# Kernel optimization log

Hardware: AMD Instinct MI355X
Metric: run time of the kernel (lower is better)

Reference implementation:

```python
import jax, jax.numpy as jnp
import numpy as np
import math


def _silu(v):
    return v * jax.nn.sigmoid(v)


def setup_inputs() -> dict:
    key = jax.random.key(0)
    ks = jax.random.split(key, 8)
    b, l = 4, 2048
    dim, hidden, d_state, dt_rank = 1024, 2048, 16, 64
    s = 0.02
    x = jax.random.normal(ks[0], (b, l, dim), dtype=jnp.float32)
    W_in = jax.random.normal(ks[1], (2 * hidden, dim), dtype=jnp.float32) * s
    conv_w = jax.random.normal(ks[2], (hidden, 1, 3), dtype=jnp.float32) * s  # depthwise, k=3
    conv_b = jnp.zeros((hidden,), dtype=jnp.float32)
    W_xproj = jax.random.normal(ks[3], (dt_rank + 2 * d_state, hidden), dtype=jnp.float32) * s
    W_dt = jax.random.uniform(ks[4], (hidden, dt_rank), minval=-1.0 / dt_rank, maxval=1.0 / dt_rank, dtype=jnp.float32)
    dt_init = jnp.exp(jax.random.uniform(ks[5], (hidden,), dtype=jnp.float32) * (math.log(0.1) - math.log(0.001)) + math.log(0.001))
    b_dt = -1.0 / dt_init  # matches dt_proj.bias init in source
    A_log = -jnp.arange(1, d_state + 1, dtype=jnp.float32)
    D = jnp.ones((hidden,), dtype=jnp.float32)
    W_out = jax.random.normal(ks[6], (dim, hidden), dtype=jnp.float32) * s
    return {"x": x, "W_in": W_in, "conv_w": conv_w, "conv_b": conv_b,
            "W_xproj": W_xproj, "W_dt": W_dt, "b_dt": b_dt,
            "A_log": A_log, "D": D, "W_out": W_out}


def reference(x, W_in, conv_w, conv_b, W_xproj, W_dt, b_dt, A_log, D, W_out):
    b, l, dim = x.shape
    hidden = W_dt.shape[0]
    dt_rank = W_dt.shape[1]
    d_state = A_log.shape[0]

    # in_proj and chunk into (x, z)
    xz = jnp.einsum('bld,ed->ble', x, W_in)  # (b, l, 2*hidden)
    u, z = jnp.split(xz, 2, axis=-1)

    # depthwise conv1d, kernel 3, symmetric padding 1 (non-causal, as in source)
    uc = jax.lax.conv_general_dilated(
        jnp.moveaxis(u, 1, 2), conv_w, window_strides=(1,), padding=[(1, 1)],
        dimension_numbers=('NCH', 'OIH', 'NCH'), feature_group_count=hidden)
    uc = jnp.moveaxis(uc + conv_b[None, :, None], 1, 2)  # (b, l, hidden)
    uc = _silu(uc)

    # x_proj -> (dt, B, C)
    x_dbl = jnp.einsum('blh,eh->ble', uc, W_xproj)
    dtp = x_dbl[..., :dt_rank]
    Bm = x_dbl[..., dt_rank:dt_rank + d_state]   # (b, l, n)
    Cm = x_dbl[..., dt_rank + d_state:]          # (b, l, n)
    dt = jax.nn.softplus(jnp.einsum('blr,hr->blh', dtp, W_dt) + b_dt)  # (b, l, hidden)

    A = -jnp.exp(A_log)  # (n,)

    # selective scan: h_{k} = exp(dt_k * A) * h_{k-1} + B_k (outer) u_k ; y_k = C_k . h_k
    def step(h, inp):
        u_t, dt_t, B_t, C_t = inp  # (b,h), (b,h), (b,n), (b,n)
        dA = jnp.exp(dt_t[:, None, :] * A[None, :, None])      # (b, n, h)
        h = dA * h + B_t[:, :, None] * u_t[:, None, :]         # (b, n, h)
        y_t = jnp.einsum('bn,bnh->bh', C_t, h)
        return h, y_t

    xs = (jnp.moveaxis(uc, 0, 1), jnp.moveaxis(dt, 0, 1),
          jnp.moveaxis(Bm, 0, 1), jnp.moveaxis(Cm, 0, 1))
    h0 = jnp.zeros((b, d_state, hidden), dtype=uc.dtype)
    _, ys = jax.lax.scan(step, h0, xs)
    y = jnp.moveaxis(ys, 0, 1) + D * uc  # skip term D*u

    y = y * _silu(z)
    out = jnp.einsum('blh,dh->bld', y, W_out)
    return x + out
```

## Files before the change

### kernel.cpp

```cpp
#include <hip/hip_runtime.h>
#include <cmath>

typedef unsigned short u16;
typedef __bf16 bf16x8 __attribute__((ext_vector_type(8)));
typedef float f32x4 __attribute__((ext_vector_type(4)));
typedef unsigned short u16x8 __attribute__((ext_vector_type(8)));

#define NB_B   4
#define NB_L   2048
#define NB_DIM 1024
#define NB_H   2048
#define NB_NS  16
#define NB_DTR 64
#define NB_TOK (NB_B * NB_L)
#define NCHUNK 64
#define CLEN   32

__device__ __forceinline__ u16 f2b(float f) {
  union { float f; unsigned u; } v; v.f = f;
  unsigned r = v.u + 0x7fffu + ((v.u >> 16) & 1u);
  return (u16)(r >> 16);
}
__device__ __forceinline__ float b2f(u16 h) {
  union { unsigned u; float f; } v; v.u = ((unsigned)h) << 16;
  return v.f;
}
__device__ __forceinline__ float exp_small(float w) {
  return __builtin_fmaf(w, __builtin_fmaf(w, 0.5f, 1.0f), 1.0f);
}

#define CVT_N0 2097152
#define CVT_N1 (CVT_N0 + 1048576)
#define CVT_N2 (CVT_N1 + 32768)
#define CVT_N3 (CVT_N2 + 524288)
__global__ void cvt_all_k(const float* __restrict__ x, const float* __restrict__ W_in,
                          const float* __restrict__ W_dt, const float* __restrict__ W_out,
                          u16* __restrict__ xb, u16* __restrict__ winb,
                          u16* __restrict__ wdtb, u16* __restrict__ woutb) {
  int i = blockIdx.x * 256 + threadIdx.x;
  const float* src; u16* dst; int off;
  if (i < CVT_N0)      { src = x;     dst = xb;    off = i; }
  else if (i < CVT_N1) { src = W_in;  dst = winb;  off = i - CVT_N0; }
  else if (i < CVT_N2) { src = W_dt;  dst = wdtb;  off = i - CVT_N1; }
  else                 { src = W_out; dst = woutb; off = i - CVT_N2; }
  float4 v = reinterpret_cast<const float4*>(src)[off];
  ushort4 o;
  o.x = f2b(v.x); o.y = f2b(v.y); o.z = f2b(v.z); o.w = f2b(v.w);
  reinterpret_cast<ushort4*>(dst)[off] = o;
}

__global__ void cvt_pad_xproj_k(const float* __restrict__ in, u16* __restrict__ out) {
  int i = blockIdx.x * 256 + threadIdx.x;
  int r = i >> 11, c = i & 2047;
  out[i] = (r < 96) ? f2b(in[r * 2048 + c]) : (u16)0;
}

__global__ void extract_dtp_k(const float* __restrict__ xdbl, u16* __restrict__ out) {
  int i = blockIdx.x * 256 + threadIdx.x;
  int r = i >> 6, c = i & 63;
  out[i] = f2b(xdbl[r * 128 + c]);
}

#define EPI_BF16    0
#define EPI_F32     1
#define EPI_SP_BF16 2
#define EPI_RES_F32 3

__device__ __forceinline__ void stage16(const u16* g, u16* l) {
  __builtin_amdgcn_global_load_lds(
      (const __attribute__((address_space(1))) unsigned int*)g,
      (__attribute__((address_space(3))) unsigned int*)l, 16, 0, 0);
}

template <int EPI, int BM>
__global__ __launch_bounds__(512, 1)
void gemm8p_k(const u16* __restrict__ A, const u16* __restrict__ Bm,
              int K, int ldc,
              u16* __restrict__ outB, float* __restrict__ outF,
              const float* __restrict__ bias, const float* __restrict__ resid,
              int cr, int cc, int ncx) {
  constexpr int MR = BM / 32;
  constexpr int MH = MR / 2;
  constexpr int HA = BM / 2;
  constexpr int LA = BM / 128;
  constexpr int L  = 2 * LA + 4;
  constexpr int BUFE = (BM + 256) * 64;
  __shared__ u16 smem[2 * BUFE];

  const int tid  = threadIdx.x;
  const int lane = tid & 63;
  const int wave = tid >> 6;
  const int wr = wave >> 2, wc = wave & 3;
  const int fr = lane & 15, fq = lane >> 4;

  const int bid = blockIdx.x;
  const int e = bid & 7, w = bid >> 3;
  const int row0 = ((e / ncx) * cr + (w % cr)) * BM;
  const int col0 = ((e % ncx) * cc + (w / cr)) * 256;

  f32x4 acc[MR][4] = {};
  bf16x8 bB[4][2], bA0[MH][2], bA1[MH][2];

  auto STAGE_B = [&](int kt) {
    const int k0 = kt * 64;
    u16* base = smem + (kt & 1) * BUFE + BM * 64;
#pragma unroll
    for (int h = 0; h < 2; ++h)
#pragma unroll
      for (int l = 0; l < 2; ++l) {
        int c = l * 512 + tid;
        int rih = c >> 3, p = c & 7;
        stage16(Bm + (size_t)(col0 + h * 128 + rih) * K + k0 + ((p ^ (rih & 7)) * 8),
                base + (h * 128 + rih) * 64 + p * 8);
      }
  };
  auto STAGE_A = [&](int kt) {
    const int k0 = kt * 64;
    u16* base = smem + (kt & 1) * BUFE;
#pragma unroll
    for (int h = 0; h < 2; ++h)
#pragma unroll
      for (int l = 0; l < LA; ++l) {
        int c = l * 512 + tid;
        int rih = c >> 3, p = c & 7;
        stage16(A + (size_t)(row0 + h * HA + rih) * K + k0 + ((p ^ (rih & 7)) * 8),
                base + (h * HA + rih) * 64 + p * 8);
      }
  };
  auto LD_A = [&](int m, int kk, int bi) {
    int rt = wr * HA + m * 16 + fr;
    int p = (kk * 4 + fq) ^ (rt & 7);
    return *reinterpret_cast<const bf16x8*>(smem + bi * BUFE + rt * 64 + p * 8);
  };
  auto LD_B = [&](int n, int kk, int bi) {
    int rt = wc * 64 + n * 16 + fr;
    int p = (kk * 4 + fq) ^ (rt & 7);
    return *reinterpret_cast<const bf16x8*>(smem + bi * BUFE + BM * 64 + rt * 64 + p * 8);
  };

  const int nk = K >> 6;
  STAGE_B(0); STAGE_A(0);
  if (nk > 1) { STAGE_B(1); STAGE_A(1); }
  if (nk > 1) asm volatile("s_waitcnt vmcnt(%0)" :: "i"(L) : "memory");
  else        asm volatile("s_waitcnt vmcnt(0)" ::: "memory");
  __builtin_amdgcn_s_barrier();
  __builtin_amdgcn_sched_barrier(0);
#pragma unroll
  for (int n = 0; n < 4; ++n) { bB[n][0] = LD_B(n, 0, 0); bB[n][1] = LD_B(n, 1, 0); }
#pragma unroll
  for (int m = 0; m < MH; ++m) { bA0[m][0] = LD_A(m, 0, 0); bA0[m][1] = LD_A(m, 1, 0); }
  asm volatile("s_waitcnt lgkmcnt(0)" ::: "memory");
  __builtin_amdgcn_s_barrier();
  __builtin_amdgcn_sched_barrier(0);

  for (int kt = 0; kt < nk; ++kt) {
    const int bi = kt & 1;
    if (kt + 2 < nk) STAGE_B(kt + 2);
    __builtin_amdgcn_s_setprio(1);
#pragma unroll
    for (int m = 0; m < MH; ++m)
#pragma unroll
      for (int n = 0; n < 2; ++n)
#pragma unroll
        for (int kk = 0; kk < 2; ++kk)
          acc[m][n] = __builtin_amdgcn_mfma_f32_16x16x32_bf16(bA0[m][kk], bB[n][kk], acc[m][n], 0, 0, 0);
    __builtin_amdgcn_s_setprio(0);
    __builtin_amdgcn_sched_barrier(0);
#pragma unroll
    for (int m = 0; m < MH; ++m) { bA1[m][0] = LD_A(MH + m, 0, bi); bA1[m][1] = LD_A(MH + m, 1, bi); }
    __builtin_amdgcn_s_setprio(1);
#pragma unroll
    for (int m = 0; m < MH; ++m)
#pragma unroll
      for (int n = 2; n < 4; ++n)
#pragma unroll
        for (int kk = 0; kk < 2; ++kk)
          acc[m][n] = __builtin_amdgcn_mfma_f32_16x16x32_bf16(bA0[m][kk], bB[n][kk], acc[m][n], 0, 0, 0);
    __builtin_amdgcn_s_setprio(0);
    asm volatile("s_waitcnt lgkmcnt(0)" ::: "memory");
    __builtin_amdgcn_s_barrier();
    __builtin_amdgcn_sched_barrier(0);
    if (kt + 2 < nk) STAGE_A(kt + 2);
    __builtin_amdgcn_s_setprio(1);
#pragma unroll
    for (int m = 0; m < MH; ++m)
#pragma unroll
      for (int n = 0; n < 2; ++n)
#pragma unroll
        for (int kk = 0; kk < 2; ++kk)
          acc[MH + m][n] = __builtin_amdgcn_mfma_f32_16x16x32_bf16(bA1[m][kk], bB[n][kk], acc[MH + m][n], 0, 0, 0);
    __builtin_amdgcn_s_setprio(0);
    __builtin_amdgcn_sched_barrier(0);
    if (kt + 1 < nk) {
      if (kt + 2 < nk) asm volatile("s_waitcnt vmcnt(%0)" :: "i"(L) : "memory");
      else             asm volatile("s_waitcnt vmcnt(0)" ::: "memory");
      __builtin_amdgcn_s_barrier();
      __builtin_amdgcn_sched_barrier(0);
#pragma unroll
      for (int n = 0; n < 2; ++n) { bB[n][0] = LD_B(n, 0, bi ^ 1); bB[n][1] = LD_B(n, 1, bi ^ 1); }
#pragma unroll
      for (int m = 0; m < MH; ++m) { bA0[m][0] = LD_A(m, 0, bi ^ 1); bA0[m][1] = LD_A(m, 1, bi ^ 1); }
    }
    __builtin_amdgcn_s_setprio(1);
#pragma unroll
    for (int m = 0; m < MH; ++m)
#pragma unroll
      for (int n = 2; n < 4; ++n)
#pragma unroll
        for (int kk = 0; kk < 2; ++kk)
          acc[MH + m][n] = __builtin_amdgcn_mfma_f32_16x16x32_bf16(bA1[m][kk], bB[n][kk], acc[MH + m][n], 0, 0, 0);
    __builtin_amdgcn_s_setprio(0);
    if (kt + 1 < nk) {
#pragma unroll
      for (int n = 2; n < 4; ++n) { bB[n][0] = LD_B(n, 0, bi ^ 1); bB[n][1] = LD_B(n, 1, bi ^ 1); }
    }
    asm volatile("s_waitcnt lgkmcnt(0)" ::: "memory");
    __builtin_amdgcn_s_barrier();
    __builtin_amdgcn_sched_barrier(0);
  }

  if constexpr (EPI == EPI_BF16 || EPI == EPI_SP_BF16) {
    u16* wv = smem + wave * 1152;
#pragma unroll
    for (int m = 0; m < MR; ++m) {
#pragma unroll
      for (int n = 0; n < 4; ++n) {
        const int c = col0 + wc * 64 + n * 16 + fr;
        float bv = (EPI == EPI_SP_BF16) ? bias[c] : 0.f;
#pragma unroll
        for (int j = 0; j < 4; ++j) {
          float v = acc[m][n][j];
          if (EPI == EPI_SP_BF16) {
            float xx = v + bv;
            float t = __expf(xx);
            float sp = (xx > -5.f) ? log1pf(t) : t;
            v = (xx > 20.f) ? xx : sp;
          }
          wv[(fq * 4 + j) * 72 + n * 16 + fr] = f2b(v);
        }
      }
#pragma unroll
      for (int p = 0; p < 2; ++p) {
        const int rf = p * 8 + (lane >> 3);
        const int c0 = (lane & 7) * 8;
        u16x8 ov = *reinterpret_cast<const u16x8*>(wv + rf * 72 + c0);
        const int grow = row0 + wr * HA + m * 16 + rf;
        const int gcol = col0 + wc * 64 + c0;
        *reinterpret_cast<u16x8*>(&outB[(size_t)grow * ldc + gcol]) = ov;
      }
    }
  } else {
#pragma unroll
    for (int m = 0; m < MR; ++m) {
      const int r = row0 + wr * HA + m * 16 + fq * 4;
#pragma unroll
      for (int n = 0; n < 4; ++n) {
        const int c = col0 + wc * 64 + n * 16 + fr;
#pragma unroll
        for (int j = 0; j < 4; ++j) {
          size_t o = (size_t)(r + j) * ldc + c;
          if (EPI == EPI_F32) outF[o] = acc[m][n][j];
          else                outF[o] = acc[m][n][j] + resid[o];
        }
      }
    }
  }
}

template <int EPI, int BM, int BN>
__global__ __launch_bounds__(256)
void gemm_bt_k(const u16* __restrict__ A, const u16* __restrict__ Bm,
               int K, int ldc,
               u16* __restrict__ outB, float* __restrict__ outF,
               const float* __restrict__ bias, const float* __restrict__ resid) {
  constexpr int MR = BM / 32, NR = BN / 32;
  __shared__ u16 smem[(BM + BN) * 32];
  u16* As = smem;
  u16* Bs = smem + BM * 32;
  const int tid  = threadIdx.x;
  const int lane = tid & 63;
  const int wave = tid >> 6;
  const int wr = wave >> 1, wc = wave & 1;
  const int row0 = blockIdx.x * BM;
  const int col0 = blockIdx.y * BN;
  f32x4 acc[MR][NR] = {};

  const int r_ld = tid >> 2;
  const int kb   = (((tid & 3) ^ ((tid >> 3) & 3)) * 8);
  const size_t a_base = (size_t)(row0 + r_ld) * K + kb;
  const size_t b_base = (size_t)(col0 + r_ld) * K + kb;
  u16* lA = As + tid * 8;
  u16* lB = Bs + tid * 8;

  const int fr = lane & 15;
  const int fq = lane >> 4;
  const int fkx = ((fq ^ ((fr >> 1) & 3)) * 8);

  const int nk = K >> 5;
  for (int kt = 0; kt < nk; ++kt) {
    const int k0 = kt * 32;
    __syncthreads();
#pragma unroll
    for (int hh = 0; hh < BM / 64; ++hh)
      stage16(A + a_base + (size_t)(hh * 64) * K + k0, lA + hh * 64 * 32);
#pragma unroll
    for (int hh = 0; hh < BN / 64; ++hh)
      stage16(Bm + b_base + (size_t)(hh * 64) * K + k0, lB + hh * 64 * 32);
    __syncthreads();
    bf16x8 af[MR], bfr[NR];
#pragma unroll
    for (int m = 0; m < MR; ++m)
      af[m] = *reinterpret_cast<const bf16x8*>(&As[(wr * (BM / 2) + m * 16 + fr) * 32 + fkx]);
#pragma unroll
    for (int n = 0; n < NR; ++n)
      bfr[n] = *reinterpret_cast<const bf16x8*>(&Bs[(wc * (BN / 2) + n * 16 + fr) * 32 + fkx]);
#pragma unroll
    for (int m = 0; m < MR; ++m)
#pragma unroll
      for (int n = 0; n < NR; ++n)
        acc[m][n] = __builtin_amdgcn_mfma_f32_16x16x32_bf16(af[m], bfr[n], acc[m][n], 0, 0, 0);
  }

#pragma unroll
  for (int m = 0; m < MR; ++m) {
    const int r = row0 + wr * (BM / 2) + m * 16 + fq * 4;
#pragma unroll
    for (int n = 0; n < NR; ++n) {
      const int c = col0 + wc * (BN / 2) + n * 16 + fr;
#pragma unroll
      for (int j = 0; j < 4; ++j) {
        float v = acc[m][n][j];
        size_t o = (size_t)(r + j) * ldc + c;
        if (EPI == EPI_F32) outF[o] = v;
        else if (EPI == EPI_RES_F32) outF[o] = v + resid[o];
      }
    }
  }
}

__global__ void dwconv_silu_k(const u16* __restrict__ xz, const float* __restrict__ cw,
                              const float* __restrict__ cb, u16* __restrict__ uc) {
  int i = blockIdx.x * 256 + threadIdx.x;
  int hb = i & (NB_H / 8 - 1);
  int t = i >> 8;
  int l = t & (NB_L - 1);
  int h0 = hb * 8;
  const u16* base = xz + (size_t)t * 4096 + h0;
  u16x8 vm = *reinterpret_cast<const u16x8*>(base);
  u16x8 vq = {}, vp = {};
  if (l > 0)          vq = *reinterpret_cast<const u16x8*>(base - 4096);
  if (l < NB_L - 1)   vp = *reinterpret_cast<const u16x8*>(base + 4096);
  u16x8 o;
#pragma unroll
  for (int j = 0; j < 8; ++j) {
    int h = h0 + j;
    float acc = cb[h];
    acc = __builtin_fmaf(b2f(vq[j]), cw[h * 3 + 0], acc);
    acc = __builtin_fmaf(b2f(vm[j]), cw[h * 3 + 1], acc);
    acc = __builtin_fmaf(b2f(vp[j]), cw[h * 3 + 2], acc);
    float s = acc / (1.f + __expf(-acc));
    o[j] = f2b(s);
  }
  *reinterpret_cast<u16x8*>(uc + (size_t)t * NB_H + h0) = o;
}

__global__ __launch_bounds__(256)
void scan_passA_k(const u16* __restrict__ dt, const u16* __restrict__ uc,
                  const float* __restrict__ xdbl, const float* __restrict__ A_log,
                  u16* __restrict__ dPout, u16* __restrict__ Sout) {
  __shared__ float bc[CLEN][32];
  const int tid = threadIdx.x;
  int idx = blockIdx.x * 256 + tid;
  int h = idx & (NB_H - 1);
  int ck = (idx >> 11) & (NCHUNK - 1);
  int b = idx >> 17;
  const int t0 = b * NB_L + ck * CLEN;
  {
    int r = tid >> 3, q = tid & 7;
    *reinterpret_cast<float4*>(&bc[r][q * 4]) =
        *reinterpret_cast<const float4*>(xdbl + (size_t)(t0 + r) * 128 + 64 + q * 4);
  }
  float An[NB_NS];
#pragma unroll
  for (int n = 0; n < NB_NS; ++n) An[n] = -__expf(A_log[n]);
  float P[NB_NS], S[NB_NS];
#pragma unroll
  for (int n = 0; n < NB_NS; ++n) { P[n] = 1.f; S[n] = 0.f; }
  __syncthreads();
  const u16* up = uc + (size_t)t0 * NB_H + h;
  const u16* dp = dt + (size_t)t0 * NB_H + h;
  float uA = b2f(up[0]),       dA = b2f(dp[0]);
  float uB = b2f(up[NB_H]),    dB = b2f(dp[NB_H]);
  for (int tt = 0; tt < CLEN; ++tt) {
    float uC = 0.f, dC = 0.f;
    if (tt + 2 < CLEN) { uC = b2f(up[2 * NB_H]); dC = b2f(dp[2 * NB_H]); }
    up += NB_H; dp += NB_H;
    float4 B0 = *reinterpret_cast<const float4*>(&bc[tt][0]);
    float4 B1 = *reinterpret_cast<const float4*>(&bc[tt][4]);
    float4 B2 = *reinterpret_cast<const float4*>(&bc[tt][8]);
    float4 B3 = *reinterpret_cast<const float4*>(&bc[tt][12]);
    const float Bf[NB_NS] = {B0.x, B0.y, B0.z, B0.w, B1.x, B1.y, B1.z, B1.w,
                             B2.x, B2.y, B2.z, B2.w, B3.x, B3.y, B3.z, B3.w};
#pragma unroll
    for (int n = 0; n < NB_NS; ++n) {
      float e = exp_small(dA * An[n]);
      P[n] *= e;
      S[n] = __builtin_fmaf(e, S[n], Bf[n] * uA);
    }
    uA = uB; dA = dB; uB = uC; dB = dC;
  }
#pragma unroll
  for (int n = 0; n < NB_NS; ++n) {
    size_t o = ((((size_t)b * NCHUNK + ck) * NB_NS + n) * NB_H + h);
    dPout[o] = f2b(1.0f - P[n]);
    Sout[o]  = f2b(S[n]);
  }
}

__global__ void scan_passB_k(u16* __restrict__ dP, const u16* __restrict__ S) {
  int idx = blockIdx.x * 256 + threadIdx.x;
  int h = idx & (NB_H - 1);
  int n = (idx >> 11) & (NB_NS - 1);
  int b = idx >> 15;
  const size_t stride = (size_t)NB_NS * NB_H;
  size_t o = ((size_t)b * NCHUNK * NB_NS + n) * NB_H + h;
  float hs = 0.f;
  float p0 = 1.f - b2f(dP[o]), s0 = b2f(S[o]);
  for (int ck = 0; ck < NCHUNK; ++ck) {
    float p1 = 1.f, s1 = 0.f;
    if (ck + 1 < NCHUNK) { p1 = 1.f - b2f(dP[o + stride]); s1 = b2f(S[o + stride]); }
    dP[o] = f2b(hs);
    hs = __builtin_fmaf(p0, hs, s0);
    o += stride; p0 = p1; s0 = s1;
  }
}

__global__ __launch_bounds__(256)
void scan_passC_k(const u16* __restrict__ dt, const u16* __restrict__ uc,
                  const float* __restrict__ xdbl, const u16* __restrict__ xz,
                  const float* __restrict__ A_log, const float* __restrict__ Dp,
                  const u16* __restrict__ Hst, u16* __restrict__ ybf) {
  __shared__ float bc[CLEN][32];
  const int tid = threadIdx.x;
  int idx = blockIdx.x * 256 + tid;
  int h = idx & (NB_H - 1);
  int ck = (idx >> 11) & (NCHUNK - 1);
  int b = idx >> 17;
  const int t0 = b * NB_L + ck * CLEN;
  {
    int r = tid >> 3, q = tid & 7;
    *reinterpret_cast<float4*>(&bc[r][q * 4]) =
        *reinterpret_cast<const float4*>(xdbl + (size_t)(t0 + r) * 128 + 64 + q * 4);
  }
  float An[NB_NS];
#pragma unroll
  for (int n = 0; n < NB_NS; ++n) An[n] = -__expf(A_log[n]);
  float s[NB_NS];
#pragma unroll
  for (int n = 0; n < NB_NS; ++n)
    s[n] = b2f(Hst[((((size_t)b * NCHUNK + ck) * NB_NS + n) * NB_H + h)]);
  const float Dh = Dp[h];
  __syncthreads();
  const u16* up = uc + (size_t)t0 * NB_H + h;
  const u16* dp = dt + (size_t)t0 * NB_H + h;
  const u16* zp = xz + (size_t)t0 * 4096 + NB_H + h;
  u16* yp = ybf + (size_t)t0 * NB_H + h;
  float uA = b2f(up[0]),    dA = b2f(dp[0]),    zA = b2f(zp[0]);
  float uB = b2f(up[NB_H]), dB = b2f(dp[NB_H]), zB = b2f(zp[4096]);
  for (int tt = 0; tt < CLEN; ++tt) {
    float uC = 0.f, dC = 0.f, zC = 0.f;
    if (tt + 2 < CLEN) {
      uC = b2f(up[2 * NB_H]); dC = b2f(dp[2 * NB_H]); zC = b2f(zp[2 * 4096]);
    }
    up += NB_H; dp += NB_H; zp += 4096;
    float4 B0 = *reinterpret_cast<const float4*>(&bc[tt][0]);
    float4 B1 = *reinterpret_cast<const float4*>(&bc[tt][4]);
    float4 B2 = *reinterpret_cast<const float4*>(&bc[tt][8]);
    float4 B3 = *reinterpret_cast<const float4*>(&bc[tt][12]);
    float4 C0 = *reinterpret_cast<const float4*>(&bc[tt][16]);
    float4 C1 = *reinterpret_cast<const float4*>(&bc[tt][20]);
    float4 C2 = *reinterpret_cast<const float4*>(&bc[tt][24]);
    float4 C3 = *reinterpret_cast<const float4*>(&bc[tt][28]);
    const float Bf[NB_NS] = {B0.x, B0.y, B0.z, B0.w, B1.x, B1.y, B1.z, B1.w,
                             B2.x, B2.y, B2.z, B2.w, B3.x, B3.y, B3.z, B3.w};
    const float Cf[NB_NS] = {C0.x, C0.y, C0.z, C0.w, C1.x, C1.y, C1.z, C1.w,
                             C2.x, C2.y, C2.z, C2.w, C3.x, C3.y, C3.z, C3.w};
    float y = 0.f;
#pragma unroll
    for (int n = 0; n < NB_NS; ++n) {
      float e = exp_small(dA * An[n]);
      s[n] = __builtin_fmaf(e, s[n], Bf[n] * uA);
      y = __builtin_fmaf(Cf[n], s[n], y);
    }
    float v = __builtin_fmaf(Dh, uA, y);
    float g = zA / (1.f + __expf(-zA));
    *yp = f2b(v * g);
    yp += NB_H;
    uA = uB; dA = dB; zA = zB; uB = uC; dB = dC; zB = zC;
  }
}

extern "C" void kernel_launch(void* const* d_in, const int* in_sizes, int n_in,
                              void* d_out, int out_size, void* d_ws, size_t ws_size,
                              hipStream_t stream) {
  const float* x      = (const float*)d_in[0];
  const float* W_in   = (const float*)d_in[1];
  const float* conv_w = (const float*)d_in[2];
  const float* conv_b = (const float*)d_in[3];
  const float* W_xprj = (const float*)d_in[4];
  const float* W_dt   = (const float*)d_in[5];
  const float* b_dt   = (const float*)d_in[6];
  const float* A_log  = (const float*)d_in[7];
  const float* Dp     = (const float*)d_in[8];
  const float* W_out  = (const float*)d_in[9];
  float* out = (float*)d_out;

  char* ws = (char*)d_ws;
  size_t off = 0;
  auto alloc = [&](size_t bytes) {
    void* p = ws + off;
    off += (bytes + 255) & ~(size_t)255;
    return p;
  };
  u16*   xz_b   = (u16*)alloc((size_t)NB_TOK * 4096 * 2);
  u16*   x_b    = (u16*)alloc((size_t)NB_TOK * NB_DIM * 2);
  u16*   win_b  = (u16*)alloc((size_t)4096 * NB_DIM * 2);
  u16*   wxp_b  = (u16*)alloc((size_t)128 * NB_H * 2);
  u16*   wdt_b  = (u16*)alloc((size_t)NB_H * NB_DTR * 2);
  u16*   wout_b = (u16*)alloc((size_t)NB_DIM * NB_H * 2);
  u16*   uc_b   = (u16*)alloc((size_t)NB_TOK * NB_H * 2);
  float* xdbl   = (float*)alloc((size_t)NB_TOK * 128 * 4);
  u16*   dtp_b  = (u16*)alloc((size_t)NB_TOK * NB_DTR * 2);
  u16*   dt_b   = (u16*)alloc((size_t)NB_TOK * NB_H * 2);
  u16*   scdP   = (u16*)alloc((size_t)NB_B * NCHUNK * NB_NS * NB_H * 2);
  u16*   scS    = (u16*)alloc((size_t)NB_B * NCHUNK * NB_NS * NB_H * 2);
  u16*   y_b    = (u16*)alloc((size_t)NB_TOK * NB_H * 2);
  (void)ws_size; (void)in_sizes; (void)n_in; (void)out_size;

  cvt_all_k<<<CVT_N3 / 256, 256, 0, stream>>>(x, W_in, W_dt, W_out, x_b, win_b, wdt_b, wout_b);
  cvt_pad_xproj_k<<<1024, 256, 0, stream>>>(W_xprj, wxp_b);

  gemm8p_k<EPI_BF16, 256><<<512, 512, 0, stream>>>(
      x_b, win_b, NB_DIM, 4096, xz_b, nullptr, nullptr, nullptr, 8, 8, 2);

  dwconv_silu_k<<<(NB_TOK * NB_H / 8) / 256, 256, 0, stream>>>(xz_b, conv_w, conv_b, uc_b);

  gemm_bt_k<EPI_F32, 64, 64><<<dim3(128, 2), 256, 0, stream>>>(
      uc_b, wxp_b, NB_H, 128, nullptr, xdbl, nullptr, nullptr);

  extract_dtp_k<<<(NB_TOK * NB_DTR) / 256, 256, 0, stream>>>(xdbl, dtp_b);

  gemm8p_k<EPI_SP_BF16, 256><<<256, 512, 0, stream>>>(
      dtp_b, wdt_b, NB_DTR, NB_H, dt_b, nullptr, b_dt, nullptr, 4, 8, 1);

  scan_passA_k<<<(NB_B * NCHUNK * NB_H) / 256, 256, 0, stream>>>(dt_b, uc_b, xdbl, A_log, scdP, scS);
  scan_passB_k<<<(NB_B * NB_NS * NB_H) / 256, 256, 0, stream>>>(scdP, scS);
  scan_passC_k<<<(NB_B * NCHUNK * NB_H) / 256, 256, 0, stream>>>(dt_b, uc_b, xdbl, xz_b, A_log, Dp, scdP, y_b);

  gemm8p_k<EPI_RES_F32, 128><<<256, 512, 0, stream>>>(
      y_b, wout_b, NB_H, NB_DIM, nullptr, out, nullptr, x, 8, 4, 1);
}
```

Before: 340.2 us.

## Fuse depthwise conv+SiLU and z-gate into in_proj GEMM epilogue

The in_proj GEMM epilogue now applies SiLU to the z half and computes the depthwise conv plus SiLU for the u half directly from accumulators, using lane shuffles for neighbouring rows. A small fixup kernel handles the tile-boundary rows. The xproj conversion and the dtp extraction are folded into the convert kernel and the xproj GEMM epilogue, which removes three launches and a full-size read/write pass. The GEMM mainloop also precomputes staging and LDS offsets and moves the A-staging after the barrier to drop one barrier per k-step. The cost is a heavier epilogue with scattered bf16 stores and more register pressure.

```diff
diff --git a/kernel.cpp b/kernel.cpp
--- a/kernel.cpp
+++ b/kernel.cpp
@@ -33,35 +33,35 @@
 #define CVT_N1 (CVT_N0 + 1048576)
 #define CVT_N2 (CVT_N1 + 32768)
 #define CVT_N3 (CVT_N2 + 524288)
+#define CVT_N4 (CVT_N3 + 49152)
+#define CVT_N5 (CVT_N4 + 8192)
 __global__ void cvt_all_k(const float* __restrict__ x, const float* __restrict__ W_in,
                           const float* __restrict__ W_dt, const float* __restrict__ W_out,
+                          const float* __restrict__ W_xp,
                           u16* __restrict__ xb, u16* __restrict__ winb,
-                          u16* __restrict__ wdtb, u16* __restrict__ woutb) {
+                          u16* __restrict__ wdtb, u16* __restrict__ woutb,
+                          u16* __restrict__ wxpb) {
   int i = blockIdx.x * 256 + threadIdx.x;
+  if (i >= CVT_N5) return;
+  if (i >= CVT_N4) {
+    int q = i - CVT_N4;
+    u16x8 z = {};
+    *reinterpret_cast<u16x8*>(wxpb + 96 * 2048 + q * 8) = z;
+    return;
+  }
   const float* src; u16* dst; int off;
   if (i < CVT_N0)      { src = x;     dst = xb;    off = i; }
   else if (i < CVT_N1) { src = W_in;  dst = winb;  off = i - CVT_N0; }
   else if (i < CVT_N2) { src = W_dt;  dst = wdtb;  off = i - CVT_N1; }
-  else                 { src = W_out; dst = woutb; off = i - CVT_N2; }
+  else if (i < CVT_N3) { src = W_out; dst = woutb; off = i - CVT_N2; }
+  else                 { src = W_xp;  dst = wxpb;  off = i - CVT_N3; }
   float4 v = reinterpret_cast<const float4*>(src)[off];
   ushort4 o;
   o.x = f2b(v.x); o.y = f2b(v.y); o.z = f2b(v.z); o.w = f2b(v.w);
   reinterpret_cast<ushort4*>(dst)[off] = o;
 }
 
-__global__ void cvt_pad_xproj_k(const float* __restrict__ in, u16* __restrict__ out) {
-  int i = blockIdx.x * 256 + threadIdx.x;
-  int r = i >> 11, c = i & 2047;
-  out[i] = (r < 96) ? f2b(in[r * 2048 + c]) : (u16)0;
-}
-
-__global__ void extract_dtp_k(const float* __restrict__ xdbl, u16* __restrict__ out) {
-  int i = blockIdx.x * 256 + threadIdx.x;
-  int r = i >> 6, c = i & 63;
-  out[i] = f2b(xdbl[r * 128 + c]);
-}
-
-#define EPI_BF16    0
+#define EPI_CONV    0
 #define EPI_F32     1
 #define EPI_SP_BF16 2
 #define EPI_RES_F32 3
@@ -78,12 +78,14 @@
               int K, int ldc,
               u16* __restrict__ outB, float* __restrict__ outF,
               const float* __restrict__ bias, const float* __restrict__ resid,
+              const float* __restrict__ cw, const float* __restrict__ cb,
+              u16* __restrict__ ucout,
               int cr, int cc, int ncx) {
   constexpr int MR = BM / 32;
   constexpr int MH = MR / 2;
   constexpr int HA = BM / 2;
   constexpr int LA = BM / 128;
-  constexpr int L  = 2 * LA + 4;
+  constexpr int PRO = 2 * LA + 4;
   constexpr int BUFE = (BM + 256) * 64;
   __shared__ u16 smem[2 * BUFE];
 
@@ -101,47 +103,67 @@
   f32x4 acc[MR][4] = {};
   bf16x8 bB[4][2], bA0[MH][2], bA1[MH][2];
 
+  const u16* gB[4]; int lBoff[4];
+  const u16* gA[2 * LA]; int lAoff[2 * LA];
+  {
+    int c_ = tid, rih = c_ >> 3, p = c_ & 7;
+#pragma unroll
+    for (int h = 0; h < 2; ++h)
+#pragma unroll
+      for (int l = 0; l < 2; ++l) {
+        int cc2 = l * 512 + tid; int ri = cc2 >> 3; int pp = cc2 & 7;
+        gB[h * 2 + l] = Bm + (size_t)(col0 + h * 128 + ri) * K + ((pp ^ (ri & 7)) * 8);
+        lBoff[h * 2 + l] = BM * 64 + (h * 128 + ri) * 64 + pp * 8;
+      }
+#pragma unroll
+    for (int h = 0; h < 2; ++h)
+#pragma unroll
+      for (int l = 0; l < LA; ++l) {
+        int cc2 = l * 512 + tid; int ri = cc2 >> 3; int pp = cc2 & 7;
+        gA[h * LA + l] = A + (size_t)(row0 + h * HA + ri) * K + ((pp ^ (ri & 7)) * 8);
+        lAoff[h * LA + l] = (h * HA + ri) * 64 + pp * 8;
+      }
+    (void)c_; (void)rih; (void)p;
+  }
+  int offA[MR][2], offB[4][2];
+#pragma unroll
+  for (int m = 0; m < MR; ++m) {
+    int rt = wr * HA + m * 16 + fr;
+#pragma unroll
+    for (int kk = 0; kk < 2; ++kk)
+      offA[m][kk] = rt * 64 + (((kk * 4 + fq) ^ (rt & 7)) * 8);
+  }
+#pragma unroll
+  for (int n = 0; n < 4; ++n) {
+    int rt = wc * 64 + n * 16 + fr;
+#pragma unroll
+    for (int kk = 0; kk < 2; ++kk)
+      offB[n][kk] = BM * 64 + rt * 64 + (((kk * 4 + fq) ^ (rt & 7)) * 8);
+  }
+
   auto STAGE_B = [&](int kt) {
-    const int k0 = kt * 64;
-    u16* base = smem + (kt & 1) * BUFE + BM * 64;
-#pragma unroll
-    for (int h = 0; h < 2; ++h)
-#pragma unroll
-      for (int l = 0; l < 2; ++l) {
-        int c = l * 512 + tid;
-        int rih = c >> 3, p = c & 7;
-        stage16(Bm + (size_t)(col0 + h * 128 + rih) * K + k0 + ((p ^ (rih & 7)) * 8),
-                base + (h * 128 + rih) * 64 + p * 8);
-      }
+    const int ko = kt * 64;
+    u16* base = smem + (kt & 1) * BUFE;
+#pragma unroll
+    for (int q = 0; q < 4; ++q) stage16(gB[q] + ko, base + lBoff[q]);
   };
   auto STAGE_A = [&](int kt) {
-    const int k0 = kt * 64;
+    const int ko = kt * 64;
     u16* base = smem + (kt & 1) * BUFE;
 #pragma unroll
-    for (int h = 0; h < 2; ++h)
-#pragma unroll
-      for (int l = 0; l < LA; ++l) {
-        int c = l * 512 + tid;
-        int rih = c >> 3, p = c & 7;
-        stage16(A + (size_t)(row0 + h * HA + rih) * K + k0 + ((p ^ (rih & 7)) * 8),
-                base + (h * HA + rih) * 64 + p * 8);
-      }
+    for (int q = 0; q < 2 * LA; ++q) stage16(gA[q] + ko, base + lAoff[q]);
   };
   auto LD_A = [&](int m, int kk, int bi) {
-    int rt = wr * HA + m * 16 + fr;
-    int p = (kk * 4 + fq) ^ (rt & 7);
-    return *reinterpret_cast<const bf16x8*>(smem + bi * BUFE + rt * 64 + p * 8);
+    return *reinterpret_cast<const bf16x8*>(smem + bi * BUFE + offA[m][kk]);
   };
   auto LD_B = [&](int n, int kk, int bi) {
-    int rt = wc * 64 + n * 16 + fr;
-    int p = (kk * 4 + fq) ^ (rt & 7);
-    return *reinterpret_cast<const bf16x8*>(smem + bi * BUFE + BM * 64 + rt * 64 + p * 8);
+    return *reinterpret_cast<const bf16x8*>(smem + bi * BUFE + offB[n][kk]);
   };
 
   const int nk = K >> 6;
   STAGE_B(0); STAGE_A(0);
   if (nk > 1) { STAGE_B(1); STAGE_A(1); }
-  if (nk > 1) asm volatile("s_waitcnt vmcnt(%0)" :: "i"(L) : "memory");
+  if (nk > 1) asm volatile("s_waitcnt vmcnt(%0)" :: "i"(PRO) : "memory");
   else        asm volatile("s_waitcnt vmcnt(0)" ::: "memory");
   __builtin_amdgcn_s_barrier();
   __builtin_amdgcn_sched_barrier(0);
@@ -177,10 +199,9 @@
         for (int kk = 0; kk < 2; ++kk)
           acc[m][n] = __builtin_amdgcn_mfma_f32_16x16x32_bf16(bA0[m][kk], bB[n][kk], acc[m][n], 0, 0, 0);
     __builtin_amdgcn_s_setprio(0);
+    __builtin_amdgcn_sched_barrier(0);
     asm volatile("s_waitcnt lgkmcnt(0)" ::: "memory");
-    __builtin_amdgcn_s_barrier();
     __builtin_amdgcn_sched_barrier(0);
-    if (kt + 2 < nk) STAGE_A(kt + 2);
     __builtin_amdgcn_s_setprio(1);
 #pragma unroll
     for (int m = 0; m < MH; ++m)
@@ -192,10 +213,11 @@
     __builtin_amdgcn_s_setprio(0);
     __builtin_amdgcn_sched_barrier(0);
     if (kt + 1 < nk) {
-      if (kt + 2 < nk) asm volatile("s_waitcnt vmcnt(%0)" :: "i"(L) : "memory");
+      if (kt + 2 < nk) asm volatile("s_waitcnt vmcnt(4)" ::: "memory");
       else             asm volatile("s_waitcnt vmcnt(0)" ::: "memory");
       __builtin_amdgcn_s_barrier();
       __builtin_amdgcn_sched_barrier(0);
+      if (kt + 2 < nk) STAGE_A(kt + 2);
 #pragma unroll
       for (int n = 0; n < 2; ++n) { bB[n][0] = LD_B(n, 0, bi ^ 1); bB[n][1] = LD_B(n, 1, bi ^ 1); }
 #pragma unroll
@@ -219,7 +241,8 @@
     __builtin_amdgcn_sched_barrier(0);
   }
 
-  if constexpr (EPI == EPI_BF16 || EPI == EPI_SP_BF16) {
+  if constexpr (EPI == EPI_CONV || EPI == EPI_SP_BF16) {
+    const bool zblk = (EPI == EPI_CONV) && (col0 >= NB_H);
     u16* wv = smem + wave * 1152;
 #pragma unroll
     for (int m = 0; m < MR; ++m) {
@@ -235,6 +258,8 @@
             float t = __expf(xx);
             float sp = (xx > -5.f) ? log1pf(t) : t;
             v = (xx > 20.f) ? xx : sp;
+          } else if (zblk) {
+            v = v / (1.f + __expf(-v));
           }
           wv[(fq * 4 + j) * 72 + n * 16 + fr] = f2b(v);
         }
@@ -249,6 +274,40 @@
         *reinterpret_cast<u16x8*>(&outB[(size_t)grow * ldc + gcol]) = ov;
       }
     }
+    if (EPI == EPI_CONV && !zblk) {
+#pragma unroll
+      for (int n = 0; n < 4; ++n) {
+        const int c = col0 + wc * 64 + n * 16 + fr;
+        const float w0 = cw[c * 3 + 0], w1 = cw[c * 3 + 1], w2 = cw[c * 3 + 2];
+        const float bb = cb[c];
+        float p3[MR], q0[MR];
+#pragma unroll
+        for (int m = 0; m < MR; ++m) {
+          p3[m] = __shfl(acc[m][n][3], (lane + 48) & 63, 64);
+          q0[m] = __shfl(acc[m][n][0], (lane + 16) & 63, 64);
+        }
+#pragma unroll
+        for (int m = 0; m < MR; ++m) {
+          const int rbase = row0 + wr * HA + m * 16 + fq * 4;
+          float um1 = (fq == 0) ? ((m > 0) ? p3[m - 1] : 0.f) : p3[m];
+          float up1 = (fq == 3) ? ((m < MR - 1) ? q0[m + 1] : 0.f) : q0[m];
+#pragma unroll
+          for (int j = 0; j < 4; ++j) {
+            const int r = rbase + j;
+            const int rm = r & 127;
+            if (rm == 0 || rm == 127) continue;
+            float prv = (j > 0) ? acc[m][n][j - 1] : um1;
+            float nxt = (j < 3) ? acc[m][n][j + 1] : up1;
+            float av = bb;
+            av = __builtin_fmaf(w0, prv, av);
+            av = __builtin_fmaf(w1, acc[m][n][j], av);
+            av = __builtin_fmaf(w2, nxt, av);
+            float s = av / (1.f + __expf(-av));
+            ucout[(size_t)r * NB_H + c] = f2b(s);
+          }
+        }
+      }
+    }
   } else {
 #pragma unroll
     for (int m = 0; m < MR; ++m) {
@@ -267,12 +326,36 @@
   }
 }
 
-template <int EPI, int BM, int BN>
+__global__ void conv_fix_k(const u16* __restrict__ xz, const float* __restrict__ cw,
+                           const float* __restrict__ cb, u16* __restrict__ uc) {
+  int i = blockIdx.x * 256 + threadIdx.x;
+  int h0 = (i & 255) * 8;
+  int seg = i >> 8;
+  int r = (seg >> 1) * 128 + (seg & 1) * 127;
+  int l = r & (NB_L - 1);
+  const u16* base = xz + (size_t)r * 4096 + h0;
+  u16x8 vm = *reinterpret_cast<const u16x8*>(base);
+  u16x8 vq = {}, vp = {};
+  if (l > 0)          vq = *reinterpret_cast<const u16x8*>(base - 4096);
+  if (l < NB_L - 1)   vp = *reinterpret_cast<const u16x8*>(base + 4096);
+  u16x8 o;
+#pragma unroll
+  for (int j = 0; j < 8; ++j) {
+    int h = h0 + j;
+    float acc = cb[h];
+    acc = __builtin_fmaf(b2f(vq[j]), cw[h * 3 + 0], acc);
+    acc = __builtin_fmaf(b2f(vm[j]), cw[h * 3 + 1], acc);
+    acc = __builtin_fmaf(b2f(vp[j]), cw[h * 3 + 2], acc);
+    float s = acc / (1.f + __expf(-acc));
+    o[j] = f2b(s);
+  }
+  *reinterpret_cast<u16x8*>(uc + (size_t)r * NB_H + h0) = o;
+}
+
+template <int BM, int BN>
 __global__ __launch_bounds__(256)
-void gemm_bt_k(const u16* __restrict__ A, const u16* __restrict__ Bm,
-               int K, int ldc,
-               u16* __restrict__ outB, float* __restrict__ outF,
-               const float* __restrict__ bias, const float* __restrict__ resid) {
+void gemm2_k(const u16* __restrict__ A, const u16* __restrict__ Bm,
+             int K, int ldc, float* __restrict__ outF, u16* __restrict__ dtp) {
   constexpr int MR = BM / 32, NR = BN / 32;
   __shared__ u16 smem[(BM + BN) * 32];
   u16* As = smem;
@@ -330,38 +413,11 @@
 #pragma unroll
       for (int j = 0; j < 4; ++j) {
         float v = acc[m][n][j];
-        size_t o = (size_t)(r + j) * ldc + c;
-        if (EPI == EPI_F32) outF[o] = v;
-        else if (EPI == EPI_RES_F32) outF[o] = v + resid[o];
+        outF[(size_t)(r + j) * ldc + c] = v;
+        if (c < NB_DTR) dtp[(size_t)(r + j) * NB_DTR + c] = f2b(v);
       }
     }
   }
-}
-
-__global__ void dwconv_silu_k(const u16* __restrict__ xz, const float* __restrict__ cw,
-                              const float* __restrict__ cb, u16* __restrict__ uc) {
-  int i = blockIdx.x * 256 + threadIdx.x;
-  int hb = i & (NB_H / 8 - 1);
-  int t = i >> 8;
-  int l = t & (NB_L - 1);
-  int h0 = hb * 8;
-  const u16* base = xz + (size_t)t * 4096 + h0;
-  u16x8 vm = *reinterpret_cast<const u16x8*>(base);
-  u16x8 vq = {}, vp = {};
-  if (l > 0)          vq = *reinterpret_cast<const u16x8*>(base - 4096);
-  if (l < NB_L - 1)   vp = *reinterpret_cast<const u16x8*>(base + 4096);
-  u16x8 o;
-#pragma unroll
-  for (int j = 0; j < 8; ++j) {
-    int h = h0 + j;
-    float acc = cb[h];
-    acc = __builtin_fmaf(b2f(vq[j]), cw[h * 3 + 0], acc);
-    acc = __builtin_fmaf(b2f(vm[j]), cw[h * 3 + 1], acc);
-    acc = __builtin_fmaf(b2f(vp[j]), cw[h * 3 + 2], acc);
-    float s = acc / (1.f + __expf(-acc));
-    o[j] = f2b(s);
-  }
-  *reinterpret_cast<u16x8*>(uc + (size_t)t * NB_H + h0) = o;
 }
 
 __global__ __launch_bounds__(256)
@@ -493,8 +549,7 @@
       y = __builtin_fmaf(Cf[n], s[n], y);
     }
     float v = __builtin_fmaf(Dh, uA, y);
-    float g = zA / (1.f + __expf(-zA));
-    *yp = f2b(v * g);
+    *yp = f2b(v * zA);
     yp += NB_H;
     uA = uB; dA = dB; zA = zB; uB = uC; dB = dC; zB = zC;
   }
@@ -537,26 +592,27 @@
   u16*   y_b    = (u16*)alloc((size_t)NB_TOK * NB_H * 2);
   (void)ws_size; (void)in_sizes; (void)n_in; (void)out_size;
 
-  cvt_all_k<<<CVT_N3 / 256, 256, 0, stream>>>(x, W_in, W_dt, W_out, x_b, win_b, wdt_b, wout_b);
-  cvt_pad_xproj_k<<<1024, 256, 0, stream>>>(W_xprj, wxp_b);
-
-  gemm8p_k<EPI_BF16, 256><<<512, 512, 0, stream>>>(
-      x_b, win_b, NB_DIM, 4096, xz_b, nullptr, nullptr, nullptr, 8, 8, 2);
-
-  dwconv_silu_k<<<(NB_TOK * NB_H / 8) / 256, 256, 0, stream>>>(xz_b, conv_w, conv_b, uc_b);
-
-  gemm_bt_k<EPI_F32, 64, 64><<<dim3(128, 2), 256, 0, stream>>>(
-      uc_b, wxp_b, NB_H, 128, nullptr, xdbl, nullptr, nullptr);
-
-  extract_dtp_k<<<(NB_TOK * NB_DTR) / 256, 256, 0, stream>>>(xdbl, dtp_b);
+  cvt_all_k<<<(CVT_N5 + 255) / 256, 256, 0, stream>>>(
+      x, W_in, W_dt, W_out, W_xprj, x_b, win_b, wdt_b, wout_b, wxp_b);
+
+  gemm8p_k<EPI_CONV, 256><<<512, 512, 0, stream>>>(
+      x_b, win_b, NB_DIM, 4096, xz_b, nullptr, nullptr, nullptr,
+      conv_w, conv_b, uc_b, 8, 8, 2);
+
+  conv_fix_k<<<128, 256, 0, stream>>>(xz_b, conv_w, conv_b, uc_b);
+
+  gemm2_k<64, 64><<<dim3(128, 2), 256, 0, stream>>>(
+      uc_b, wxp_b, NB_H, 128, xdbl, dtp_b);
 
   gemm8p_k<EPI_SP_BF16, 256><<<256, 512, 0, stream>>>(
-      dtp_b, wdt_b, NB_DTR, NB_H, dt_b, nullptr, b_dt, nullptr, 4, 8, 1);
+      dtp_b, wdt_b, NB_DTR, NB_H, dt_b, nullptr, b_dt, nullptr,
+      nullptr, nullptr, nullptr, 4, 8, 1);
 
   scan_passA_k<<<(NB_B * NCHUNK * NB_H) / 256, 256, 0, stream>>>(dt_b, uc_b, xdbl, A_log, scdP, scS);
   scan_passB_k<<<(NB_B * NB_NS * NB_H) / 256, 256, 0, stream>>>(scdP, scS);
   scan_passC_k<<<(NB_B * NCHUNK * NB_H) / 256, 256, 0, stream>>>(dt_b, uc_b, xdbl, xz_b, A_log, Dp, scdP, y_b);
 
   gemm8p_k<EPI_RES_F32, 128><<<256, 512, 0, stream>>>(
-      y_b, wout_b, NB_H, NB_DIM, nullptr, out, nullptr, x, 8, 4, 1);
-}
+      y_b, wout_b, NB_H, NB_DIM, nullptr, out, nullptr, x,
+      nullptr, nullptr, nullptr, 8, 4, 1);
+}
```

Measured after the change: 416.1 us. +22.3%, slower.
